# Kernel tuning notes

Hardware: AMD Instinct MI355X
Metric: run time of the kernel (lower is better)

## Reference

```python
import jax, jax.numpy as jnp
import numpy as np

N_TOKENS = 7168
EMBED_DIM = 256
N_HEADS = 8
HEAD_DIM = EMBED_DIM // N_HEADS  # 32
HALF = HEAD_DIM // 2             # 16 rotary frequency pairs per head
BATCH = 4
MAX_LEN = 2048
POSITION_DIM = 2
N_LEVELS = 4
LN_EPS = 1e-5
SPATIAL_THETA = 100.0
LEVEL_THETA = 10.0


def setup_inputs() -> dict:
    key = jax.random.key(0)
    ks = jax.random.split(key, 6)
    x = jax.random.normal(ks[0], (N_TOKENS, EMBED_DIM), jnp.float32)
    level_indices = jax.random.randint(ks[1], (N_TOKENS,), 0, N_LEVELS, dtype=jnp.int32)
    level_spatial_shapes = jnp.array([[32, 32], [16, 16], [8, 8], [4, 4]], jnp.int32)
    # positions in each token's own level coordinate space
    u = jax.random.uniform(ks[2], (N_TOKENS, POSITION_DIM), jnp.float32)
    spatial_positions = u * level_spatial_shapes[level_indices].astype(jnp.float32)
    # ragged batch boundaries: lengths [2048, 1536, 2048, 1536]
    batch_offsets = jnp.array([0, 2048, 3584, 5632, 7168], jnp.int32)
    ln_w = jnp.ones((EMBED_DIM,), jnp.float32)
    ln_b = jnp.zeros((EMBED_DIM,), jnp.float32)
    qkv_w = jax.random.normal(ks[3], (3 * EMBED_DIM, EMBED_DIM), jnp.float32) * (EMBED_DIM ** -0.5)
    out_w = jax.random.normal(ks[4], (EMBED_DIM, EMBED_DIM), jnp.float32) * (EMBED_DIM ** -0.5)
    # ND-RoPE frequencies: (position_dim+1, n_heads, head_dim//2).
    # Spatial dims share magnitude theta_s^(-i/HALF) split over a random per-head
    # direction angle; level dim uses theta_l^(-i/HALF).
    mag_s = SPATIAL_THETA ** (-jnp.arange(HALF, dtype=jnp.float32) / HALF)
    mag_l = LEVEL_THETA ** (-jnp.arange(HALF, dtype=jnp.float32) / HALF)
    phi = jax.random.uniform(ks[5], (N_HEADS, HALF), jnp.float32) * (2.0 * jnp.pi)
    freqs = jnp.stack([mag_s * jnp.cos(phi),
                       mag_s * jnp.sin(phi),
                       jnp.broadcast_to(mag_l, (N_HEADS, HALF))], axis=0)
    return {"x": x, "spatial_positions": spatial_positions,
            "level_indices": level_indices, "level_spatial_shapes": level_spatial_shapes,
            "batch_offsets": batch_offsets, "ln_w": ln_w, "ln_b": ln_b,
            "qkv_w": qkv_w, "out_w": out_w, "freqs": freqs}


def reference(x, spatial_positions, level_indices, level_spatial_shapes,
              batch_offsets, ln_w, ln_b, qkv_w, out_w, freqs):
    residual = x
    # pre-norm LayerNorm
    mu = jnp.mean(x, -1, keepdims=True)
    var = jnp.mean((x - mu) ** 2, -1, keepdims=True)
    xn = (x - mu) * jax.lax.rsqrt(var + LN_EPS) * ln_w + ln_b
    q, k, v = jnp.split(xn @ qkv_w.T, 3, axis=-1)  # each (N, E)
    # prep_multilevel_positions: rescale each level to the max level's coordinate
    # frame and append the level index as an extra position dim.
    shapes_tok = level_spatial_shapes[level_indices].astype(jnp.float32)  # (N, 2)
    max_shape = jnp.max(level_spatial_shapes, axis=0).astype(jnp.float32)  # (2,)
    pos = jnp.concatenate([spatial_positions * (max_shape / shapes_tok),
                           level_indices[:, None].astype(jnp.float32)], axis=-1)  # (N, 3)
    # per-head ND RoPE: angle = sum_d pos_d * freq_d
    theta = jnp.einsum('nd,dhf->nhf', pos, freqs)  # (N, H, HALF)
    cos, sin = jnp.cos(theta), jnp.sin(theta)

    def rope(t):
        t = t.reshape(N_TOKENS, N_HEADS, HALF, 2)
        r = jnp.stack([t[..., 0] * cos - t[..., 1] * sin,
                       t[..., 0] * sin + t[..., 1] * cos], axis=-1)
        return r.reshape(N_TOKENS, EMBED_DIM)

    q, k = rope(q), rope(k)
    # concatenated -> padded (B, S, E)
    tok = jnp.arange(N_TOKENS)
    b_of = jnp.searchsorted(batch_offsets, tok, side='right') - 1  # (N,) batch index
    p_of = tok - batch_offsets[b_of]                               # (N,) pos in batch
    lens = batch_offsets[1:] - batch_offsets[:-1]
    pad_mask = jnp.arange(MAX_LEN)[None, :] >= lens[:, None]  # (B, S), True = padding

    def heads(t):
        padded = jnp.zeros((BATCH, MAX_LEN, EMBED_DIM), t.dtype).at[b_of, p_of].set(t)
        return padded.reshape(BATCH, MAX_LEN, N_HEADS, HEAD_DIM).transpose(0, 2, 1, 3)

    qh, kh, vh = heads(q), heads(k), heads(v)  # (B, H, S, hd)
    scores = jnp.einsum('bhqd,bhkd->bhqk', qh, kh) / np.float32(np.sqrt(HEAD_DIM))
    scores = jnp.where(pad_mask[:, None, None, :], jnp.float32(-1e9), scores)
    attn = jax.nn.softmax(scores, axis=-1)
    out = jnp.einsum('bhqk,bhkd->bhqd', attn, vh)
    out = out.transpose(0, 2, 1, 3).reshape(BATCH, MAX_LEN, EMBED_DIM)
    out_cat = out[b_of, p_of]  # padded -> concatenated (padded rows dropped)
    return out_cat @ out_w.T + residual
```

## Files before the change

### kernel.cpp

```cpp
#include <hip/hip_runtime.h>
#include <hip/hip_bf16.h>

#define NT   7168
#define ED   256
#define NH   8
#define HD   32
#define HF   16
#define QKVN 768
#define QSCL 0.25503471600819466f

typedef float f32x4  __attribute__((ext_vector_type(4)));
typedef __bf16 bf16x8 __attribute__((ext_vector_type(8)));

__device__ __forceinline__ short f2bf(float f) {
    union { float f; unsigned u; } v; v.f = f;
    unsigned r = v.u + 0x7FFFu + ((v.u >> 16) & 1u);
    return (short)(r >> 16);
}
__device__ __forceinline__ float fexp2(float x) {
    float r; asm("v_exp_f32 %0, %1" : "=v"(r) : "v"(x)); return r;
}
__device__ __forceinline__ unsigned cvtpk(float lo, float hi) {
    unsigned r; asm("v_cvt_pk_bf16_f32 %0, %1, %2" : "=v"(r) : "v"(lo), "v"(hi)); return r;
}
__device__ __forceinline__ float bf2f(short s) {
    union { unsigned u; float f; } v; v.u = ((unsigned)(unsigned short)s) << 16;
    return v.f;
}
__device__ __forceinline__ void gll16(const void* g, void* l) {
    __builtin_amdgcn_global_load_lds((const __attribute__((address_space(1))) void*)g,
                                     (__attribute__((address_space(3))) void*)l, 16, 0, 0);
}

__global__ __launch_bounds__(256) void ln_conv_kernel(const float* __restrict__ x,
                                                      const float* __restrict__ w,
                                                      const float* __restrict__ b,
                                                      short* __restrict__ xn,
                                                      const float* __restrict__ qkvw,
                                                      const float* __restrict__ outw,
                                                      short* __restrict__ wq,
                                                      short* __restrict__ wo) {
    int bid = blockIdx.x;
    if (bid >= NT / 4) {
        int i = (bid - NT / 4) * 256 + threadIdx.x;
        if (i < QKVN * ED) wq[i] = f2bf(qkvw[i]);
        if (i < ED * ED)   wo[i] = f2bf(outw[i]);
        return;
    }
    int tok  = bid * 4 + (threadIdx.x >> 6);
    int lane = threadIdx.x & 63;
    const float4 xv = *reinterpret_cast<const float4*>(x + tok * ED + lane * 4);
    float s  = xv.x + xv.y + xv.z + xv.w;
    float ss = xv.x * xv.x + xv.y * xv.y + xv.z * xv.z + xv.w * xv.w;
#pragma unroll
    for (int m = 1; m < 64; m <<= 1) { s += __shfl_xor(s, m); ss += __shfl_xor(ss, m); }
    float mu  = s * (1.0f / ED);
    float inv = rsqrtf(ss * (1.0f / ED) - mu * mu + 1e-5f);
    const float4 wv = *reinterpret_cast<const float4*>(w + lane * 4);
    const float4 bv = *reinterpret_cast<const float4*>(b + lane * 4);
    short4 o;
    o.x = f2bf((xv.x - mu) * inv * wv.x + bv.x);
    o.y = f2bf((xv.y - mu) * inv * wv.y + bv.y);
    o.z = f2bf((xv.z - mu) * inv * wv.z + bv.z);
    o.w = f2bf((xv.w - mu) * inv * wv.w + bv.w);
    *reinterpret_cast<short4*>(xn + tok * ED + lane * 4) = o;
}

__global__ __launch_bounds__(256) void gemm_qkv(const short* __restrict__ A,
                                                const short* __restrict__ B,
                                                short* __restrict__ C) {
    int wv = threadIdx.x >> 6, lane = threadIdx.x & 63;
    int r = lane & 15, g = lane >> 4;
    int mt = blockIdx.x * 128 + wv * 32;
    int jt = blockIdx.y * 64;
    const short* arow0 = A + (mt + r) * ED + g * 8;
    const short* arow1 = A + (mt + 16 + r) * ED + g * 8;
    const short* brow  = B + (jt + r) * ED + g * 8;
    f32x4 acc0[4] = {{0,0,0,0},{0,0,0,0},{0,0,0,0},{0,0,0,0}};
    f32x4 acc1[4] = {{0,0,0,0},{0,0,0,0},{0,0,0,0},{0,0,0,0}};
#pragma unroll
    for (int k0 = 0; k0 < ED; k0 += 32) {
        bf16x8 a0 = *reinterpret_cast<const bf16x8*>(arow0 + k0);
        bf16x8 a1 = *reinterpret_cast<const bf16x8*>(arow1 + k0);
#pragma unroll
        for (int c = 0; c < 4; ++c) {
            bf16x8 bb = *reinterpret_cast<const bf16x8*>(brow + c * 16 * ED + k0);
            acc0[c] = __builtin_amdgcn_mfma_f32_16x16x32_bf16(a0, bb, acc0[c], 0, 0, 0);
            acc1[c] = __builtin_amdgcn_mfma_f32_16x16x32_bf16(a1, bb, acc1[c], 0, 0, 0);
        }
    }
#pragma unroll
    for (int c = 0; c < 4; ++c)
#pragma unroll
        for (int rr = 0; rr < 4; ++rr) {
            C[(mt + g * 4 + rr) * QKVN + jt + c * 16 + r]      = f2bf(acc0[c][rr]);
            C[(mt + 16 + g * 4 + rr) * QKVN + jt + c * 16 + r] = f2bf(acc1[c][rr]);
        }
}

__global__ __launch_bounds__(256) void gemm_out(const short* __restrict__ A,
                                                const short* __restrict__ B,
                                                const float* __restrict__ res,
                                                float* __restrict__ out) {
    int wv = threadIdx.x >> 6, lane = threadIdx.x & 63;
    int r = lane & 15, g = lane >> 4;
    int mt = blockIdx.x * 64 + wv * 16;
    int jt = blockIdx.y * 64;
    const short* arow = A + (mt + r) * ED + g * 8;
    const short* brow = B + (jt + r) * ED + g * 8;
    f32x4 acc[4] = {{0,0,0,0},{0,0,0,0},{0,0,0,0},{0,0,0,0}};
#pragma unroll
    for (int k0 = 0; k0 < ED; k0 += 32) {
        bf16x8 a = *reinterpret_cast<const bf16x8*>(arow + k0);
#pragma unroll
        for (int c = 0; c < 4; ++c) {
            bf16x8 bb = *reinterpret_cast<const bf16x8*>(brow + c * 16 * ED + k0);
            acc[c] = __builtin_amdgcn_mfma_f32_16x16x32_bf16(a, bb, acc[c], 0, 0, 0);
        }
    }
#pragma unroll
    for (int c = 0; c < 4; ++c)
#pragma unroll
        for (int rr = 0; rr < 4; ++rr) {
            int idx = (mt + g * 4 + rr) * ED + jt + c * 16 + r;
            out[idx] = acc[c][rr] + res[idx];
        }
}

__global__ __launch_bounds__(256) void rope_vt_kernel(short* __restrict__ qkv,
                                                      const float* __restrict__ sp,
                                                      const int* __restrict__ lvl,
                                                      const int* __restrict__ shp,
                                                      const float* __restrict__ freqs,
                                                      short* __restrict__ vt) {
    int bid = blockIdx.x;
    if (bid >= NT * NH * HF / 256) {
        __shared__ short tile[32][72];
        int b2 = bid - NT * NH * HF / 256;
        int t0 = (b2 >> 3) * 64, h = b2 & 7;
        int tid = threadIdx.x;
#pragma unroll
        for (int rep = 0; rep < 8; ++rep) {
            int idx = rep * 256 + tid;
            int t_in = idx >> 5, d = idx & 31;
            tile[d][t_in] = qkv[(t0 + t_in) * QKVN + 2 * ED + h * HD + d];
        }
        __syncthreads();
#pragma unroll
        for (int rep = 0; rep < 8; ++rep) {
            int idx = rep * 256 + tid;
            int d = idx >> 6, s = idx & 63;
            int pm = (s & 32) | ((s & 4) << 2) | ((s & 24) >> 1) | (s & 3);
            vt[(h * HD + d) * NT + t0 + s] = tile[d][pm];
        }
        return;
    }
    int idx = bid * 256 + threadIdx.x;
    int t = idx >> 7, h = (idx >> 4) & 7, f = idx & 15;
    int L = lvl[t];
    float mx0 = fmaxf(fmaxf((float)shp[0], (float)shp[2]), fmaxf((float)shp[4], (float)shp[6]));
    float mx1 = fmaxf(fmaxf((float)shp[1], (float)shp[3]), fmaxf((float)shp[5], (float)shp[7]));
    float p0 = sp[t * 2]     * (mx0 / (float)shp[L * 2]);
    float p1 = sp[t * 2 + 1] * (mx1 / (float)shp[L * 2 + 1]);
    float p2 = (float)L;
    float th = p0 * freqs[(0 * NH + h) * HF + f]
             + p1 * freqs[(1 * NH + h) * HF + f]
             + p2 * freqs[(2 * NH + h) * HF + f];
    float sn, cs;
    __sincosf(th, &sn, &cs);
    short* qp = qkv + t * QKVN + h * HD + 2 * f;
    float a0 = bf2f(qp[0]), a1 = bf2f(qp[1]);
    qp[0] = f2bf((a0 * cs - a1 * sn) * QSCL);
    qp[1] = f2bf((a0 * sn + a1 * cs) * QSCL);
    short* kp = qp + ED;
    float b0 = bf2f(kp[0]), b1 = bf2f(kp[1]);
    kp[0] = f2bf(b0 * cs - b1 * sn);
    kp[1] = f2bf(b0 * sn + b1 * cs);
}

__global__ __launch_bounds__(256) void attn_kernel(const short* __restrict__ qkv,
                                                   const short* __restrict__ vt,
                                                   short* __restrict__ obf) {
    __shared__ __align__(16) short smem[16384];
    const int tid = threadIdx.x;
    const int wv = tid >> 6, lane = tid & 63;
    const int bid = blockIdx.x;
    const int h = bid & 7, pr = bid >> 3;
    const int b = (pr >= 32) + (pr >= 56) + (pr >= 88);
    const int off = (b == 0) ? 0 : (b == 1) ? 2048 : (b == 2) ? 3584 : 5632;
    const int len = (b == 0) ? 2048 : (b == 1) ? 1536 : (b == 2) ? 2048 : 1536;
    const int pb  = (b == 0) ? 0 : (b == 1) ? 32 : (b == 2) ? 56 : 88;
    const int q0 = off + (pr - pb) * 64;
    const int r = lane & 15, g = lane >> 4;
    const int qi = wv & 1, half = wv >> 1;
    const int hl = len >> 1;
    const int nst = hl >> 6;
    const int qs = q0 + qi * 32;

    const short* pK = qkv + ED + h * HD + (size_t)(off + (tid >> 2)) * QKVN + (tid & 3) * 8;
    const short* pV = vt + (size_t)(h * HD + ((tid >> 2) & 31)) * NT + off + (tid >> 7) * 32 + (tid & 3) * 8;
    const int hlK = hl * QKVN;

#define STAGE(B, s) { \
        const short* a_ = pK + (size_t)(s) * 64 * QKVN; \
        gll16(a_,       &smem[(B) * 8192 +        tid * 8]); \
        gll16(a_ + hlK, &smem[(B) * 8192 + 2048 + tid * 8]); \
        const short* v_ = pV + (s) * 64; \
        gll16(v_,       &smem[(B) * 8192 + 4096 + tid * 8]); \
        gll16(v_ + hl,  &smem[(B) * 8192 + 6144 + tid * 8]); }

    bf16x8 qfA = *reinterpret_cast<const bf16x8*>(qkv + (size_t)(qs + r) * QKVN + h * HD + g * 8);
    bf16x8 qfB = *reinterpret_cast<const bf16x8*>(qkv + (size_t)(qs + 16 + r) * QKVN + h * HD + g * 8);
    union { unsigned u[4]; bf16x8 v; } onesu;
    onesu.u[0] = onesu.u[1] = onesu.u[2] = onesu.u[3] = 0x3F803F80u;
    const bf16x8 ones = onesu.v;

    f32x4 o0A = {0,0,0,0}, o1A = {0,0,0,0}, o0B = {0,0,0,0}, o1B = {0,0,0,0};
    f32x4 olA = {0,0,0,0}, olB = {0,0,0,0};

    STAGE(0, 0);
    __syncthreads();

    for (int st = 0; st < nst; ++st) {
        const int B = st & 1;
        if (st + 1 < nst) STAGE(B ^ 1, st + 1);
        const short* kl = &smem[B * 8192 + half * 2048];
        const short* vl = &smem[B * 8192 + 4096 + half * 2048];
        bf16x8 kf0 = *reinterpret_cast<const bf16x8*>(kl +        r * 32 + g * 8);
        bf16x8 kf1 = *reinterpret_cast<const bf16x8*>(kl +  512 + r * 32 + g * 8);
        bf16x8 kf2 = *reinterpret_cast<const bf16x8*>(kl + 1024 + r * 32 + g * 8);
        bf16x8 kf3 = *reinterpret_cast<const bf16x8*>(kl + 1536 + r * 32 + g * 8);
        bf16x8 v00 = *reinterpret_cast<const bf16x8*>(vl +        r * 32 + g * 8);
        bf16x8 v10 = *reinterpret_cast<const bf16x8*>(vl +  512 + r * 32 + g * 8);
        bf16x8 v01 = *reinterpret_cast<const bf16x8*>(vl + 1024 + r * 32 + g * 8);
        bf16x8 v11 = *reinterpret_cast<const bf16x8*>(vl + 1536 + r * 32 + g * 8);

        const f32x4 z = {0, 0, 0, 0};
        f32x4 sA0 = __builtin_amdgcn_mfma_f32_16x16x32_bf16(kf0, qfA, z, 0, 0, 0);
        f32x4 sA1 = __builtin_amdgcn_mfma_f32_16x16x32_bf16(kf1, qfA, z, 0, 0, 0);
        f32x4 sA2 = __builtin_amdgcn_mfma_f32_16x16x32_bf16(kf2, qfA, z, 0, 0, 0);
        f32x4 sA3 = __builtin_amdgcn_mfma_f32_16x16x32_bf16(kf3, qfA, z, 0, 0, 0);
        f32x4 sB0 = __builtin_amdgcn_mfma_f32_16x16x32_bf16(kf0, qfB, z, 0, 0, 0);
        f32x4 sB1 = __builtin_amdgcn_mfma_f32_16x16x32_bf16(kf1, qfB, z, 0, 0, 0);
        f32x4 sB2 = __builtin_amdgcn_mfma_f32_16x16x32_bf16(kf2, qfB, z, 0, 0, 0);
        f32x4 sB3 = __builtin_amdgcn_mfma_f32_16x16x32_bf16(kf3, qfB, z, 0, 0, 0);

#pragma unroll
        for (int i = 0; i < 4; ++i) {
            sA0[i] = fexp2(sA0[i]); sA1[i] = fexp2(sA1[i]);
            sA2[i] = fexp2(sA2[i]); sA3[i] = fexp2(sA3[i]);
            sB0[i] = fexp2(sB0[i]); sB1[i] = fexp2(sB1[i]);
            sB2[i] = fexp2(sB2[i]); sB3[i] = fexp2(sB3[i]);
        }
        union { unsigned u[4]; bf16x8 v; } pA0, pA1, pB0, pB1;
        pA0.u[0] = cvtpk(sA0[0], sA0[1]); pA0.u[1] = cvtpk(sA0[2], sA0[3]);
        pA0.u[2] = cvtpk(sA1[0], sA1[1]); pA0.u[3] = cvtpk(sA1[2], sA1[3]);
        pA1.u[0] = cvtpk(sA2[0], sA2[1]); pA1.u[1] = cvtpk(sA2[2], sA2[3]);
        pA1.u[2] = cvtpk(sA3[0], sA3[1]); pA1.u[3] = cvtpk(sA3[2], sA3[3]);
        pB0.u[0] = cvtpk(sB0[0], sB0[1]); pB0.u[1] = cvtpk(sB0[2], sB0[3]);
        pB0.u[2] = cvtpk(sB1[0], sB1[1]); pB0.u[3] = cvtpk(sB1[2], sB1[3]);
        pB1.u[0] = cvtpk(sB2[0], sB2[1]); pB1.u[1] = cvtpk(sB2[2], sB2[3]);
        pB1.u[2] = cvtpk(sB3[0], sB3[1]); pB1.u[3] = cvtpk(sB3[2], sB3[3]);
        o0A = __builtin_amdgcn_mfma_f32_16x16x32_bf16(v00, pA0.v, o0A, 0, 0, 0);
        o0A = __builtin_amdgcn_mfma_f32_16x16x32_bf16(v01, pA1.v, o0A, 0, 0, 0);
        o1A = __builtin_amdgcn_mfma_f32_16x16x32_bf16(v10, pA0.v, o1A, 0, 0, 0);
        o1A = __builtin_amdgcn_mfma_f32_16x16x32_bf16(v11, pA1.v, o1A, 0, 0, 0);
        o0B = __builtin_amdgcn_mfma_f32_16x16x32_bf16(v00, pB0.v, o0B, 0, 0, 0);
        o0B = __builtin_amdgcn_mfma_f32_16x16x32_bf16(v01, pB1.v, o0B, 0, 0, 0);
        o1B = __builtin_amdgcn_mfma_f32_16x16x32_bf16(v10, pB0.v, o1B, 0, 0, 0);
        o1B = __builtin_amdgcn_mfma_f32_16x16x32_bf16(v11, pB1.v, o1B, 0, 0, 0);
        olA = __builtin_amdgcn_mfma_f32_16x16x32_bf16(ones, pA0.v, olA, 0, 0, 0);
        olA = __builtin_amdgcn_mfma_f32_16x16x32_bf16(ones, pA1.v, olA, 0, 0, 0);
        olB = __builtin_amdgcn_mfma_f32_16x16x32_bf16(ones, pB0.v, olB, 0, 0, 0);
        olB = __builtin_amdgcn_mfma_f32_16x16x32_bf16(ones, pB1.v, olB, 0, 0, 0);
        __syncthreads();
    }

    float lA = olA[0], lB = olB[0];

    float* cf = (float*)smem + (qi * 64 + lane) * 19;
    if (half) {
#pragma unroll
        for (int i = 0; i < 4; ++i) {
            cf[i] = o0A[i]; cf[4 + i] = o1A[i]; cf[8 + i] = o0B[i]; cf[12 + i] = o1B[i];
        }
        cf[16] = lA; cf[17] = lB;
    }
    __syncthreads();
    if (!half) {
        lA += cf[16]; lB += cf[17];
#pragma unroll
        for (int i = 0; i < 4; ++i) {
            o0A[i] += cf[i];     o1A[i] += cf[4 + i];
            o0B[i] += cf[8 + i]; o1B[i] += cf[12 + i];
        }
        float iA = 1.f / lA, iB = 1.f / lB;
        short4 w;
        short* orowA = obf + (qs + r) * ED + h * HD;
        w.x = f2bf(o0A[0] * iA); w.y = f2bf(o0A[1] * iA);
        w.z = f2bf(o0A[2] * iA); w.w = f2bf(o0A[3] * iA);
        *reinterpret_cast<short4*>(orowA + g * 4) = w;
        w.x = f2bf(o1A[0] * iA); w.y = f2bf(o1A[1] * iA);
        w.z = f2bf(o1A[2] * iA); w.w = f2bf(o1A[3] * iA);
        *reinterpret_cast<short4*>(orowA + 16 + g * 4) = w;
        short* orowB = obf + (qs + 16 + r) * ED + h * HD;
        w.x = f2bf(o0B[0] * iB); w.y = f2bf(o0B[1] * iB);
        w.z = f2bf(o0B[2] * iB); w.w = f2bf(o0B[3] * iB);
        *reinterpret_cast<short4*>(orowB + g * 4) = w;
        w.x = f2bf(o1B[0] * iB); w.y = f2bf(o1B[1] * iB);
        w.z = f2bf(o1B[2] * iB); w.w = f2bf(o1B[3] * iB);
        *reinterpret_cast<short4*>(orowB + 16 + g * 4) = w;
    }
#undef STAGE
}

extern "C" void kernel_launch(void* const* d_in, const int* in_sizes, int n_in,
                              void* d_out, int out_size, void* d_ws, size_t ws_size,
                              hipStream_t stream) {
    const float* x     = (const float*)d_in[0];
    const float* sp    = (const float*)d_in[1];
    const int*   lvl   = (const int*)d_in[2];
    const int*   shp   = (const int*)d_in[3];
    const float* lnw   = (const float*)d_in[5];
    const float* lnb   = (const float*)d_in[6];
    const float* qkvw  = (const float*)d_in[7];
    const float* outw  = (const float*)d_in[8];
    const float* freqs = (const float*)d_in[9];
    float* out = (float*)d_out;

    char* ws = (char*)d_ws;
    short* xn  = (short*)ws; ws += NT * ED * 2;
    short* qkv = (short*)ws; ws += NT * QKVN * 2;
    short* vt  = (short*)ws; ws += ED * NT * 2;
    short* obf = (short*)ws; ws += NT * ED * 2;
    short* wq  = (short*)ws; ws += QKVN * ED * 2;
    short* wo  = (short*)ws; ws += ED * ED * 2;

    ln_conv_kernel<<<dim3(NT / 4 + 768), dim3(256), 0, stream>>>(x, lnw, lnb, xn,
                                                                 qkvw, outw, wq, wo);
    gemm_qkv<<<dim3(NT / 128, QKVN / 64), dim3(256), 0, stream>>>(xn, wq, qkv);
    rope_vt_kernel<<<dim3(NT * NH * HF / 256 + NT / 64 * NH), dim3(256), 0, stream>>>(
        qkv, sp, lvl, shp, freqs, vt);
    attn_kernel<<<dim3(112 * 8), dim3(256), 0, stream>>>(qkv, vt, obf);
    gemm_out<<<dim3(NT / 64, ED / 64), dim3(256), 0, stream>>>(obf, wo, x, out);
}
```

Before: 72.22 us.

## Fuse RoPE and V transpose into QKV GEMM epilogue, precompute sin/cos table

Computes the per-token rotary cos/sin table inside the layernorm kernel and stores it as packed bf16. The QKV GEMM epilogue then applies RoPE and the Q scale to Q/K, and writes V directly in transposed, permuted layout. This removes the separate rope/V-transpose kernel launch and its extra pass over qkv. It also adds s_setprio around the MFMA bursts in attention. In exchange, the table is stored in bf16 (lower precision for cos/sin), the epilogue does scattered vt stores, and the epilogue has extra shuffles and table loads.

```diff
diff --git a/kernel.cpp b/kernel.cpp
--- a/kernel.cpp
+++ b/kernel.cpp
@@ -27,6 +27,10 @@
     union { unsigned u; float f; } v; v.u = ((unsigned)(unsigned short)s) << 16;
     return v.f;
 }
+__device__ __forceinline__ unsigned pack2bf(float a, float b) {
+    union { float f; unsigned u; } ua, ub; ua.f = a; ub.f = b;
+    return ((ua.u + 0x8000u) >> 16) | ((ub.u + 0x8000u) & 0xFFFF0000u);
+}
 __device__ __forceinline__ void gll16(const void* g, void* l) {
     __builtin_amdgcn_global_load_lds((const __attribute__((address_space(1))) void*)g,
                                      (__attribute__((address_space(3))) void*)l, 16, 0, 0);
@@ -39,16 +43,22 @@
                                                       const float* __restrict__ qkvw,
                                                       const float* __restrict__ outw,
                                                       short* __restrict__ wq,
-                                                      short* __restrict__ wo) {
+                                                      short* __restrict__ wo,
+                                                      const float* __restrict__ sp,
+                                                      const int* __restrict__ lvl,
+                                                      const int* __restrict__ shp,
+                                                      const float* __restrict__ freqs,
+                                                      unsigned* __restrict__ tab) {
     int bid = blockIdx.x;
+    int tid = threadIdx.x;
     if (bid >= NT / 4) {
-        int i = (bid - NT / 4) * 256 + threadIdx.x;
+        int i = (bid - NT / 4) * 256 + tid;
         if (i < QKVN * ED) wq[i] = f2bf(qkvw[i]);
         if (i < ED * ED)   wo[i] = f2bf(outw[i]);
         return;
     }
-    int tok  = bid * 4 + (threadIdx.x >> 6);
-    int lane = threadIdx.x & 63;
+    int tok  = bid * 4 + (tid >> 6);
+    int lane = tid & 63;
     const float4 xv = *reinterpret_cast<const float4*>(x + tok * ED + lane * 4);
     float s  = xv.x + xv.y + xv.z + xv.w;
     float ss = xv.x * xv.x + xv.y * xv.y + xv.z * xv.z + xv.w * xv.w;
@@ -64,11 +74,33 @@
     o.z = f2bf((xv.z - mu) * inv * wv.z + bv.z);
     o.w = f2bf((xv.w - mu) * inv * wv.w + bv.w);
     *reinterpret_cast<short4*>(xn + tok * ED + lane * 4) = o;
+
+    int tt = bid * 4 + (tid >> 6);
+    int h  = (tid >> 3) & 7;
+    int f  = (tid & 7) * 2;
+    int L = lvl[tt];
+    float mx0 = fmaxf(fmaxf((float)shp[0], (float)shp[2]), fmaxf((float)shp[4], (float)shp[6]));
+    float mx1 = fmaxf(fmaxf((float)shp[1], (float)shp[3]), fmaxf((float)shp[5], (float)shp[7]));
+    float p0 = sp[tt * 2]     * (mx0 / (float)shp[L * 2]);
+    float p1 = sp[tt * 2 + 1] * (mx1 / (float)shp[L * 2 + 1]);
+    float p2 = (float)L;
+    int fi = h * HF + f;
+    float th0 = p0 * freqs[fi]       + p1 * freqs[128 + fi]       + p2 * freqs[256 + fi];
+    float th1 = p0 * freqs[fi + 1]   + p1 * freqs[128 + fi + 1]   + p2 * freqs[256 + fi + 1];
+    float sn0, cs0, sn1, cs1;
+    __sincosf(th0, &sn0, &cs0);
+    __sincosf(th1, &sn1, &cs1);
+    uint2 pk;
+    pk.x = pack2bf(cs0, sn0);
+    pk.y = pack2bf(cs1, sn1);
+    *reinterpret_cast<uint2*>(&tab[tt * 128 + fi]) = pk;
 }
 
 __global__ __launch_bounds__(256) void gemm_qkv(const short* __restrict__ A,
                                                 const short* __restrict__ B,
-                                                short* __restrict__ C) {
+                                                short* __restrict__ C,
+                                                const unsigned* __restrict__ tab,
+                                                short* __restrict__ vt) {
     int wv = threadIdx.x >> 6, lane = threadIdx.x & 63;
     int r = lane & 15, g = lane >> 4;
     int mt = blockIdx.x * 128 + wv * 32;
@@ -89,13 +121,50 @@
             acc1[c] = __builtin_amdgcn_mfma_f32_16x16x32_bf16(a1, bb, acc1[c], 0, 0, 0);
         }
     }
-#pragma unroll
-    for (int c = 0; c < 4; ++c)
-#pragma unroll
-        for (int rr = 0; rr < 4; ++rr) {
-            C[(mt + g * 4 + rr) * QKVN + jt + c * 16 + r]      = f2bf(acc0[c][rr]);
-            C[(mt + 16 + g * 4 + rr) * QKVN + jt + c * 16 + r] = f2bf(acc1[c][rr]);
-        }
+    if (jt < 512) {
+        const float qs = (jt < 256) ? QSCL : 1.0f;
+        const int sgn = r & 1;
+#pragma unroll
+        for (int c = 0; c < 4; ++c) {
+            int col = jt + c * 16 + r;
+            int hf = ((col >> 5) & 7) * 16 + ((col >> 1) & 15);
+#pragma unroll
+            for (int rr = 0; rr < 4; ++rr) {
+                int t0 = mt + g * 4 + rr;
+                {
+                    unsigned pk = tab[t0 * 128 + hf];
+                    float cs = bf2f((short)(pk & 0xFFFF)), sn = bf2f((short)(pk >> 16));
+                    float v = acc0[c][rr], p = __shfl_xor(v, 1);
+                    float o = sgn ? (v * cs + p * sn) : (v * cs - p * sn);
+                    C[t0 * QKVN + col] = f2bf(o * qs);
+                }
+                {
+                    int t1 = t0 + 16;
+                    unsigned pk = tab[t1 * 128 + hf];
+                    float cs = bf2f((short)(pk & 0xFFFF)), sn = bf2f((short)(pk >> 16));
+                    float v = acc1[c][rr], p = __shfl_xor(v, 1);
+                    float o = sgn ? (v * cs + p * sn) : (v * cs - p * sn);
+                    C[t1 * QKVN + col] = f2bf(o * qs);
+                }
+            }
+        }
+    } else {
+#pragma unroll
+        for (int c = 0; c < 4; ++c) {
+            int dg = jt - 512 + c * 16 + r;
+#pragma unroll
+            for (int rr = 0; rr < 4; ++rr) {
+                int t0 = mt + g * 4 + rr;
+                int u0 = t0 & 63;
+                int s0 = (u0 & 35) | ((u0 & 12) << 1) | ((u0 & 16) >> 2);
+                vt[dg * NT + (t0 & ~63) + s0] = f2bf(acc0[c][rr]);
+                int t1 = t0 + 16;
+                int u1 = t1 & 63;
+                int s1 = (u1 & 35) | ((u1 & 12) << 1) | ((u1 & 16) >> 2);
+                vt[dg * NT + (t1 & ~63) + s1] = f2bf(acc1[c][rr]);
+            }
+        }
+    }
 }
 
 __global__ __launch_bounds__(256) void gemm_out(const short* __restrict__ A,
@@ -125,57 +194,6 @@
             int idx = (mt + g * 4 + rr) * ED + jt + c * 16 + r;
             out[idx] = acc[c][rr] + res[idx];
         }
-}
-
-__global__ __launch_bounds__(256) void rope_vt_kernel(short* __restrict__ qkv,
-                                                      const float* __restrict__ sp,
-                                                      const int* __restrict__ lvl,
-                                                      const int* __restrict__ shp,
-                                                      const float* __restrict__ freqs,
-                                                      short* __restrict__ vt) {
-    int bid = blockIdx.x;
-    if (bid >= NT * NH * HF / 256) {
-        __shared__ short tile[32][72];
-        int b2 = bid - NT * NH * HF / 256;
-        int t0 = (b2 >> 3) * 64, h = b2 & 7;
-        int tid = threadIdx.x;
-#pragma unroll
-        for (int rep = 0; rep < 8; ++rep) {
-            int idx = rep * 256 + tid;
-            int t_in = idx >> 5, d = idx & 31;
-            tile[d][t_in] = qkv[(t0 + t_in) * QKVN + 2 * ED + h * HD + d];
-        }
-        __syncthreads();
-#pragma unroll
-        for (int rep = 0; rep < 8; ++rep) {
-            int idx = rep * 256 + tid;
-            int d = idx >> 6, s = idx & 63;
-            int pm = (s & 32) | ((s & 4) << 2) | ((s & 24) >> 1) | (s & 3);
-            vt[(h * HD + d) * NT + t0 + s] = tile[d][pm];
-        }
-        return;
-    }
-    int idx = bid * 256 + threadIdx.x;
-    int t = idx >> 7, h = (idx >> 4) & 7, f = idx & 15;
-    int L = lvl[t];
-    float mx0 = fmaxf(fmaxf((float)shp[0], (float)shp[2]), fmaxf((float)shp[4], (float)shp[6]));
-    float mx1 = fmaxf(fmaxf((float)shp[1], (float)shp[3]), fmaxf((float)shp[5], (float)shp[7]));
-    float p0 = sp[t * 2]     * (mx0 / (float)shp[L * 2]);
-    float p1 = sp[t * 2 + 1] * (mx1 / (float)shp[L * 2 + 1]);
-    float p2 = (float)L;
-    float th = p0 * freqs[(0 * NH + h) * HF + f]
-             + p1 * freqs[(1 * NH + h) * HF + f]
-             + p2 * freqs[(2 * NH + h) * HF + f];
-    float sn, cs;
-    __sincosf(th, &sn, &cs);
-    short* qp = qkv + t * QKVN + h * HD + 2 * f;
-    float a0 = bf2f(qp[0]), a1 = bf2f(qp[1]);
-    qp[0] = f2bf((a0 * cs - a1 * sn) * QSCL);
-    qp[1] = f2bf((a0 * sn + a1 * cs) * QSCL);
-    short* kp = qp + ED;
-    float b0 = bf2f(kp[0]), b1 = bf2f(kp[1]);
-    kp[0] = f2bf(b0 * cs - b1 * sn);
-    kp[1] = f2bf(b0 * sn + b1 * cs);
 }
 
 __global__ __launch_bounds__(256) void attn_kernel(const short* __restrict__ qkv,
@@ -236,6 +254,7 @@
         bf16x8 v11 = *reinterpret_cast<const bf16x8*>(vl + 1536 + r * 32 + g * 8);
 
         const f32x4 z = {0, 0, 0, 0};
+        __builtin_amdgcn_s_setprio(1);
         f32x4 sA0 = __builtin_amdgcn_mfma_f32_16x16x32_bf16(kf0, qfA, z, 0, 0, 0);
         f32x4 sA1 = __builtin_amdgcn_mfma_f32_16x16x32_bf16(kf1, qfA, z, 0, 0, 0);
         f32x4 sA2 = __builtin_amdgcn_mfma_f32_16x16x32_bf16(kf2, qfA, z, 0, 0, 0);
@@ -244,6 +263,7 @@
         f32x4 sB1 = __builtin_amdgcn_mfma_f32_16x16x32_bf16(kf1, qfB, z, 0, 0, 0);
         f32x4 sB2 = __builtin_amdgcn_mfma_f32_16x16x32_bf16(kf2, qfB, z, 0, 0, 0);
         f32x4 sB3 = __builtin_amdgcn_mfma_f32_16x16x32_bf16(kf3, qfB, z, 0, 0, 0);
+        __builtin_amdgcn_s_setprio(0);
 
 #pragma unroll
         for (int i = 0; i < 4; ++i) {
@@ -261,6 +281,7 @@
         pB0.u[2] = cvtpk(sB1[0], sB1[1]); pB0.u[3] = cvtpk(sB1[2], sB1[3]);
         pB1.u[0] = cvtpk(sB2[0], sB2[1]); pB1.u[1] = cvtpk(sB2[2], sB2[3]);
         pB1.u[2] = cvtpk(sB3[0], sB3[1]); pB1.u[3] = cvtpk(sB3[2], sB3[3]);
+        __builtin_amdgcn_s_setprio(1);
         o0A = __builtin_amdgcn_mfma_f32_16x16x32_bf16(v00, pA0.v, o0A, 0, 0, 0);
         o0A = __builtin_amdgcn_mfma_f32_16x16x32_bf16(v01, pA1.v, o0A, 0, 0, 0);
         o1A = __builtin_amdgcn_mfma_f32_16x16x32_bf16(v10, pA0.v, o1A, 0, 0, 0);
@@ -273,6 +294,7 @@
         olA = __builtin_amdgcn_mfma_f32_16x16x32_bf16(ones, pA1.v, olA, 0, 0, 0);
         olB = __builtin_amdgcn_mfma_f32_16x16x32_bf16(ones, pB0.v, olB, 0, 0, 0);
         olB = __builtin_amdgcn_mfma_f32_16x16x32_bf16(ones, pB1.v, olB, 0, 0, 0);
+        __builtin_amdgcn_s_setprio(0);
         __syncthreads();
     }
 
@@ -335,12 +357,11 @@
     short* obf = (short*)ws; ws += NT * ED * 2;
     short* wq  = (short*)ws; ws += QKVN * ED * 2;
     short* wo  = (short*)ws; ws += ED * ED * 2;
-
-    ln_conv_kernel<<<dim3(NT / 4 + 768), dim3(256), 0, stream>>>(x, lnw, lnb, xn,
-                                                                 qkvw, outw, wq, wo);
-    gemm_qkv<<<dim3(NT / 128, QKVN / 64), dim3(256), 0, stream>>>(xn, wq, qkv);
-    rope_vt_kernel<<<dim3(NT * NH * HF / 256 + NT / 64 * NH), dim3(256), 0, stream>>>(
-        qkv, sp, lvl, shp, freqs, vt);
+    unsigned* tab = (unsigned*)ws; ws += NT * 128 * 4;
+
+    ln_conv_kernel<<<dim3(NT / 4 + 768), dim3(256), 0, stream>>>(
+        x, lnw, lnb, xn, qkvw, outw, wq, wo, sp, lvl, shp, freqs, tab);
+    gemm_qkv<<<dim3(NT / 128, QKVN / 64), dim3(256), 0, stream>>>(xn, wq, qkv, tab, vt);
     attn_kernel<<<dim3(112 * 8), dim3(256), 0, stream>>>(qkv, vt, obf);
     gemm_out<<<dim3(NT / 64, ED / 64), dim3(256), 0, stream>>>(obf, wo, x, out);
 }
```

New measurement: 68.36 us. -5.3%, faster.
